# Performance work log

Measured on AMD Instinct MI355X. Metric: run time of the kernel, lower is better.

Reference implementation:

```python
import jax, jax.numpy as jnp
import numpy as np

EMBED = 512
HEADS = 8
HEAD_DIM = EMBED // HEADS


def setup_inputs() -> dict:
    key = jax.random.key(0)
    ks = jax.random.split(key, 11)
    B, S, E = 2, 4096, EMBED
    scale = 1.0 / np.sqrt(E)
    inp = {
        "q": jax.random.normal(ks[0], (B, S, E), dtype=jnp.float32),
        "k": jax.random.normal(ks[1], (B, S, E), dtype=jnp.float32),
        "v": jax.random.normal(ks[2], (B, S, E), dtype=jnp.float32),
        # linear layer params (torch nn.Linear: y = x @ W.T + b)
        "Wq": jax.random.normal(ks[3], (E, E), dtype=jnp.float32) * scale,
        "bq": jnp.zeros((E,), dtype=jnp.float32),
        "Wk": jax.random.normal(ks[4], (E, E), dtype=jnp.float32) * scale,
        "bk": jnp.zeros((E,), dtype=jnp.float32),
        "Wv": jax.random.normal(ks[5], (E, E), dtype=jnp.float32) * scale,
        "bv": jnp.zeros((E,), dtype=jnp.float32),
        "Wo": jax.random.normal(ks[6], (E, E), dtype=jnp.float32) * scale,
        "bo": jnp.zeros((E,), dtype=jnp.float32),
    }
    return inp


def reference(q, k, v, Wq, bq, Wk, bk, Wv, bv, Wo, bo):
    B, Sq, E = q.shape
    Sk = k.shape[1]
    H, D = HEADS, HEAD_DIM
    # projections, split heads: [B, S, H, D]
    qh = (q @ Wq.T + bq).reshape(B, Sq, H, D)
    kh = (k @ Wk.T + bk).reshape(B, Sk, H, D)
    vh = (v @ Wv.T + bv).reshape(B, Sk, H, D)
    # full score matrix [B, H, Sq, Sk]; note: scaled by sqrt(embed_size), matching source
    scores = jnp.einsum('bqhe,bkhe->bhqk', qh, kh) / jnp.sqrt(jnp.float32(E))
    probs = jax.nn.softmax(scores, axis=-1)
    attn = jnp.einsum('bhql,blhd->bqhd', probs, vh)  # [B, Sq, H, D]
    concat = attn.reshape(B, Sq, E)
    return concat @ Wo.T + bo
```

## Files before the change

kernel.cpp:

```cpp
#include <hip/hip_runtime.h>
#include <hip/hip_bf16.h>

#define DEVFN __device__ __forceinline__

typedef __attribute__((ext_vector_type(8))) __bf16 bf16x8;
typedef __attribute__((ext_vector_type(4))) float f32x4;
typedef __attribute__((ext_vector_type(16))) float f32x16;

constexpr int E  = 512;
constexpr int S  = 4096;
constexpr int HD = 64;
constexpr int RT = 8192;

DEVFN unsigned int cvt_pk_bf16(float lo, float hi) {
  unsigned int r;
  asm("v_cvt_pk_bf16_f32 %0, %1, %2" : "=v"(r) : "v"(lo), "v"(hi));
  return r;
}
DEVFN void plswap(unsigned int& a, unsigned int& b) {
  asm("v_permlane32_swap_b32 %0, %1" : "+v"(a), "+v"(b));
}
DEVFN float ex2(float x) { return __builtin_amdgcn_exp2f(x); }

DEVFN unsigned short f2bf(float f) {
  union { float f; unsigned int u; } v; v.f = f;
  unsigned int u = v.u;
  return (unsigned short)((u + 0x7fffu + ((u >> 16) & 1u)) >> 16);
}

DEVFN f32x4 mfma16(bf16x8 a, bf16x8 b, f32x4 c) {
  return __builtin_amdgcn_mfma_f32_16x16x32_bf16(a, b, c, 0, 0, 0);
}
DEVFN f32x16 mfma32(bf16x8 a, bf16x8 b, f32x16 c) {
  return __builtin_amdgcn_mfma_f32_32x32x16_bf16(a, b, c, 0, 0, 0);
}

DEVFN uint4 pk8(const float4& a, const float4& b) {
  uint4 r;
  r.x = cvt_pk_bf16(a.x, a.y); r.y = cvt_pk_bf16(a.z, a.w);
  r.z = cvt_pk_bf16(b.x, b.y); r.w = cvt_pk_bf16(b.z, b.w);
  return r;
}
DEVFN bf16x8 asbf(uint4 u) { union { uint4 a; bf16x8 b; } c; c.a = u; return c.b; }

template<typename TIN, int OMODE>
DEVFN void gemm_body(const TIN* __restrict__ X, const float* __restrict__ W,
                     const float* __restrict__ bias, void* __restrict__ outp,
                     float scale, unsigned short (*Al)[72], unsigned short (*Bl)[72]) {
  const int bid0 = blockIdx.x;
  const int bid = ((bid0 & 7) << 5) | (bid0 >> 3);
  const int bm = bid >> 2, bn = bid & 3;
  const int tid = threadIdx.x;
  const int w = tid >> 6, lane = tid & 63;
  const int g = lane >> 4, ln = lane & 15;
  const int wm = w >> 2, wn = w & 3;
  const int r0 = bm * 128, n0 = bn * 128;
  const int srw = tid >> 2, sc0 = (tid & 3) * 16;

  f32x4 acc[4][2] = {};

  float4 af[4];
  uint4  au[2];
  float4 bp[4];

  auto loadA = [&](int k0) {
    if constexpr (sizeof(TIN) == 4) {
      const float* src = (const float*)X + (size_t)(r0 + srw) * E + k0 + sc0;
      #pragma unroll
      for (int i = 0; i < 4; ++i) af[i] = *(const float4*)(src + i * 4);
    } else {
      const unsigned short* src = (const unsigned short*)X + (size_t)(r0 + srw) * E + k0 + sc0;
      #pragma unroll
      for (int i = 0; i < 2; ++i) au[i] = *(const uint4*)(src + i * 8);
    }
  };
  auto loadB = [&](int k0) {
    const float* src = W + (size_t)(n0 + srw) * E + k0 + sc0;
    #pragma unroll
    for (int i = 0; i < 4; ++i) bp[i] = *(const float4*)(src + i * 4);
  };

  loadA(0); loadB(0);

  for (int k0 = 0; k0 < E; k0 += 64) {
    if constexpr (sizeof(TIN) == 4) {
      *(uint4*)&Al[srw][sc0]     = pk8(af[0], af[1]);
      *(uint4*)&Al[srw][sc0 + 8] = pk8(af[2], af[3]);
    } else {
      *(uint4*)&Al[srw][sc0]     = au[0];
      *(uint4*)&Al[srw][sc0 + 8] = au[1];
    }
    *(uint4*)&Bl[srw][sc0]     = pk8(bp[0], bp[1]);
    *(uint4*)&Bl[srw][sc0 + 8] = pk8(bp[2], bp[3]);
    __syncthreads();
    if (k0 + 64 < E) { loadA(k0 + 64); loadB(k0 + 64); }

    __builtin_amdgcn_s_setprio(1);
    #pragma unroll
    for (int kk = 0; kk < 2; ++kk) {
      bf16x8 afr[4], bfr[2];
      #pragma unroll
      for (int i = 0; i < 4; ++i)
        afr[i] = *(const bf16x8*)&Al[wm*64 + i*16 + ln][kk*32 + 8*g];
      #pragma unroll
      for (int j = 0; j < 2; ++j)
        bfr[j] = *(const bf16x8*)&Bl[wn*32 + j*16 + ln][kk*32 + 8*g];
      #pragma unroll
      for (int i = 0; i < 4; ++i)
        #pragma unroll
        for (int j = 0; j < 2; ++j)
          acc[i][j] = mfma16(afr[i], bfr[j], acc[i][j]);
    }
    __builtin_amdgcn_s_setprio(0);
    __syncthreads();
  }

  #pragma unroll
  for (int j = 0; j < 2; ++j) {
    const int gcol = n0 + wn*32 + j*16 + ln;
    const float bv = bias[gcol];
    #pragma unroll
    for (int i = 0; i < 4; ++i) {
      const int gr = r0 + wm*64 + i*16 + 4*g;
      #pragma unroll
      for (int r = 0; r < 4; ++r) {
        const float v = (acc[i][j][r] + bv) * scale;
        if constexpr (OMODE == 1)
          ((float*)outp)[(size_t)(gr + r) * E + gcol] = v;
        else if constexpr (OMODE == 0)
          ((unsigned short*)outp)[(size_t)(gr + r) * E + gcol] = f2bf(v);
        else
          ((unsigned short*)outp)[((size_t)((gr + r) >> 12) * E + gcol) * S + ((gr + r) & (S - 1))] = f2bf(v);
      }
    }
  }
}

__global__ __launch_bounds__(512) void gemm_qkv(const float* __restrict__ q,
    const float* __restrict__ k, const float* __restrict__ v,
    const float* __restrict__ Wq, const float* __restrict__ bq,
    const float* __restrict__ Wk, const float* __restrict__ bk,
    const float* __restrict__ Wv, const float* __restrict__ bv,
    unsigned short* qh, unsigned short* kh, unsigned short* vhT, float qscale) {
  __shared__ unsigned short Al[128][72];
  __shared__ unsigned short Bl[128][72];
  const int y = blockIdx.y;
  if (y == 0)      gemm_body<float, 0>(q, Wq, bq, qh, qscale, Al, Bl);
  else if (y == 1) gemm_body<float, 0>(k, Wk, bk, kh, 1.0f, Al, Bl);
  else             gemm_body<float, 2>(v, Wv, bv, vhT, 1.0f, Al, Bl);
}

__global__ __launch_bounds__(512) void gemm_o(const unsigned short* __restrict__ cc,
    const float* __restrict__ Wo, const float* __restrict__ bo, float* out) {
  __shared__ unsigned short Al[128][72];
  __shared__ unsigned short Bl[128][72];
  gemm_body<unsigned short, 1>(cc, Wo, bo, out, 1.0f, Al, Bl);
}

__global__ __launch_bounds__(512) void attn_fwd(const unsigned short* __restrict__ qh,
                                                const unsigned short* __restrict__ kh,
                                                const unsigned short* __restrict__ vhT,
                                                unsigned short* __restrict__ cc) {
  __shared__ unsigned short SM[4][64][72];

  const int bid = blockIdx.x;
  const int swz = (bid & 7) * 64 + (bid >> 3);
  const int bh = swz >> 5, qt = swz & 31;
  const int b = bh >> 3, h = bh & 7;

  const int tid = threadIdx.x;
  const int wv = tid >> 6, lane = tid & 63;
  const int half = wv >> 2, w4 = wv & 3;
  const int l31 = lane & 31, hi = lane >> 5;

  unsigned short (*K_lds)[72] = SM[2*half];
  unsigned short (*V_lds)[72] = SM[2*half + 1];

  const unsigned short* qb = qh + (size_t)b * S * E + h * HD;
  const unsigned short* kb = kh + (size_t)b * S * E + h * HD;
  const unsigned short* vb = vhT + ((size_t)b * E + h * HD) * S;
  const int q0 = qt * 128 + w4 * 32;
  const int tbase = half * (S / 2);

  bf16x8 qf[4];
  #pragma unroll
  for (int kf = 0; kf < 4; ++kf)
    qf[kf] = *(const bf16x8*)(qb + (size_t)(q0 + l31) * E + kf*16 + 8*hi);

  f32x16 o0 = {}, o1 = {};
  float ml = -__builtin_inff(), ll = 0.f;

  const int t256 = tid & 255;
  const int srow = t256 >> 2, sc0 = (t256 & 3) * 16;
  const unsigned short* kS = kb + (size_t)(tbase + srow) * E + sc0;
  const unsigned short* vS = vb + (size_t)srow * S + tbase + sc0;

  uint4 kr0 = *(const uint4*)kS, kr1 = *(const uint4*)(kS + 8);
  uint4 vr0 = *(const uint4*)vS, vr1 = *(const uint4*)(vS + 8);

  constexpr int NIT = S / 2 / 64;
  for (int it = 0; it < NIT; ++it) {
    *(uint4*)&K_lds[srow][sc0]     = kr0;
    *(uint4*)&K_lds[srow][sc0 + 8] = kr1;
    *(uint4*)&V_lds[srow][sc0]     = vr0;
    *(uint4*)&V_lds[srow][sc0 + 8] = vr1;
    __syncthreads();

    if (it + 1 < NIT) {
      const unsigned short* kp = kS + (size_t)(it + 1) * 64 * E;
      const unsigned short* vp = vS + (it + 1) * 64;
      kr0 = *(const uint4*)kp; kr1 = *(const uint4*)(kp + 8);
      vr0 = *(const uint4*)vp; vr1 = *(const uint4*)(vp + 8);
    }

    f32x16 s0 = {}, s1 = {};
    __builtin_amdgcn_s_setprio(1);
    #pragma unroll
    for (int kf = 0; kf < 4; ++kf) {
      bf16x8 ka = *(const bf16x8*)&K_lds[l31]     [kf*16 + 8*hi];
      bf16x8 kc = *(const bf16x8*)&K_lds[32 + l31][kf*16 + 8*hi];
      s0 = mfma32(ka, qf[kf], s0);
      s1 = mfma32(kc, qf[kf], s1);
    }
    __builtin_amdgcn_s_setprio(0);

    float tm = -__builtin_inff();
    #pragma unroll
    for (int r = 0; r < 16; ++r) tm = fmaxf(tm, fmaxf(s0[r], s1[r]));
    tm = fmaxf(tm, __shfl_xor(tm, 32));

    if (!__all(tm <= ml + 8.f)) {
      const float mn = fmaxf(ml, tm);
      const float fr = ex2(ml - mn);
      ml = mn; ll *= fr;
      #pragma unroll
      for (int r = 0; r < 16; ++r) { o0[r] *= fr; o1[r] *= fr; }
    }

    float rs = 0.f;
    #pragma unroll
    for (int r = 0; r < 16; ++r) {
      s0[r] = ex2(s0[r] - ml); rs += s0[r];
      s1[r] = ex2(s1[r] - ml); rs += s1[r];
    }
    rs += __shfl_xor(rs, 32);
    ll += rs;

    unsigned int a0 = cvt_pk_bf16(s0[0],  s0[1]),  a1 = cvt_pk_bf16(s0[2],  s0[3]);
    unsigned int a2 = cvt_pk_bf16(s0[4],  s0[5]),  a3 = cvt_pk_bf16(s0[6],  s0[7]);
    unsigned int a4 = cvt_pk_bf16(s0[8],  s0[9]),  a5 = cvt_pk_bf16(s0[10], s0[11]);
    unsigned int a6 = cvt_pk_bf16(s0[12], s0[13]), a7 = cvt_pk_bf16(s0[14], s0[15]);
    plswap(a0, a2); plswap(a1, a3); plswap(a4, a6); plswap(a5, a7);
    unsigned int c0 = cvt_pk_bf16(s1[0],  s1[1]),  c1 = cvt_pk_bf16(s1[2],  s1[3]);
    unsigned int c2 = cvt_pk_bf16(s1[4],  s1[5]),  c3 = cvt_pk_bf16(s1[6],  s1[7]);
    unsigned int c4 = cvt_pk_bf16(s1[8],  s1[9]),  c5 = cvt_pk_bf16(s1[10], s1[11]);
    unsigned int c6 = cvt_pk_bf16(s1[12], s1[13]), c7 = cvt_pk_bf16(s1[14], s1[15]);
    plswap(c0, c2); plswap(c1, c3); plswap(c4, c6); plswap(c5, c7);
    uint4 pa[4];
    pa[0] = uint4{a0, a1, a2, a3};
    pa[1] = uint4{a4, a5, a6, a7};
    pa[2] = uint4{c0, c1, c2, c3};
    pa[3] = uint4{c4, c5, c6, c7};

    __builtin_amdgcn_s_setprio(1);
    #pragma unroll
    for (int tf = 0; tf < 4; ++tf) {
      bf16x8 va = *(const bf16x8*)&V_lds[l31]     [tf*16 + 8*hi];
      bf16x8 vc = *(const bf16x8*)&V_lds[32 + l31][tf*16 + 8*hi];
      bf16x8 pf = asbf(pa[tf]);
      o0 = mfma32(va, pf, o0);
      o1 = mfma32(vc, pf, o1);
    }
    __builtin_amdgcn_s_setprio(0);
    __syncthreads();
  }

  float* cb = (float*)SM;
  float* p = cb + (size_t)(w4 * 64 + lane) * 34;
  if (half) {
    #pragma unroll
    for (int r = 0; r < 16; ++r) { p[r] = o0[r]; p[16 + r] = o1[r]; }
    p[32] = ml; p[33] = ll;
  }
  __syncthreads();
  if (!half) {
    const float m2 = p[32], l2 = p[33];
    const float m = fmaxf(ml, m2);
    const float f1 = ex2(ml - m), f2 = ex2(m2 - m);
    ll = ll * f1 + l2 * f2;
    #pragma unroll
    for (int r = 0; r < 16; ++r) {
      o0[r] = o0[r] * f1 + p[r] * f2;
      o1[r] = o1[r] * f1 + p[16 + r] * f2;
    }

    const float inv = 1.0f / ll;
    const size_t rowb = (size_t)(b * S + q0 + l31) * E + h * HD;
    #pragma unroll
    for (int qd = 0; qd < 4; ++qd) {
      uint2 w0, w1;
      w0.x = cvt_pk_bf16(o0[4*qd]     * inv, o0[4*qd + 1] * inv);
      w0.y = cvt_pk_bf16(o0[4*qd + 2] * inv, o0[4*qd + 3] * inv);
      *(uint2*)&cc[rowb + 8*qd + 4*hi] = w0;
      w1.x = cvt_pk_bf16(o1[4*qd]     * inv, o1[4*qd + 1] * inv);
      w1.y = cvt_pk_bf16(o1[4*qd + 2] * inv, o1[4*qd + 3] * inv);
      *(uint2*)&cc[rowb + 32 + 8*qd + 4*hi] = w1;
    }
  }
}

extern "C" void kernel_launch(void* const* d_in, const int* in_sizes, int n_in,
                              void* d_out, int out_size, void* d_ws, size_t ws_size,
                              hipStream_t stream) {
  const float* q  = (const float*)d_in[0];
  const float* k  = (const float*)d_in[1];
  const float* v  = (const float*)d_in[2];
  const float* Wq = (const float*)d_in[3];
  const float* bq = (const float*)d_in[4];
  const float* Wk = (const float*)d_in[5];
  const float* bk = (const float*)d_in[6];
  const float* Wv = (const float*)d_in[7];
  const float* bv = (const float*)d_in[8];
  const float* Wo = (const float*)d_in[9];
  const float* bo = (const float*)d_in[10];
  float* out = (float*)d_out;

  unsigned short* qh  = (unsigned short*)d_ws;
  unsigned short* kh  = qh + (size_t)RT * E;
  unsigned short* vhT = kh + (size_t)RT * E;
  unsigned short* cc  = vhT + (size_t)RT * E;

  const float qscale = 1.4426950408889634f / 22.62741699796952f;

  gemm_qkv<<<dim3(256, 3), dim3(512), 0, stream>>>(q, k, v, Wq, bq, Wk, bk, Wv, bv,
                                                   qh, kh, vhT, qscale);
  attn_fwd<<<dim3(512), dim3(512), 0, stream>>>(qh, kh, vhT, cc);
  gemm_o<<<dim3(256), dim3(512), 0, stream>>>(cc, Wo, bo, out);
}
```

Before: 144.0 us.

## Split KV tile into 32-key subtiles and fold max subtraction into MFMA accumulator init

```diff
diff --git a/kernel.cpp b/kernel.cpp
--- a/kernel.cpp
+++ b/kernel.cpp
@@ -188,7 +188,8 @@
     qf[kf] = *(const bf16x8*)(qb + (size_t)(q0 + l31) * E + kf*16 + 8*hi);
 
   f32x16 o0 = {}, o1 = {};
-  float ml = -__builtin_inff(), ll = 0.f;
+  f32x16 cml = {};
+  float ml = 0.f, ll = 0.f;
 
   const int t256 = tid & 255;
   const int srow = t256 >> 2, sc0 = (t256 & 3) * 16;
@@ -213,65 +214,67 @@
       vr0 = *(const uint4*)vp; vr1 = *(const uint4*)(vp + 8);
     }
 
-    f32x16 s0 = {}, s1 = {};
-    __builtin_amdgcn_s_setprio(1);
-    #pragma unroll
-    for (int kf = 0; kf < 4; ++kf) {
-      bf16x8 ka = *(const bf16x8*)&K_lds[l31]     [kf*16 + 8*hi];
-      bf16x8 kc = *(const bf16x8*)&K_lds[32 + l31][kf*16 + 8*hi];
-      s0 = mfma32(ka, qf[kf], s0);
-      s1 = mfma32(kc, qf[kf], s1);
-    }
-    __builtin_amdgcn_s_setprio(0);
-
-    float tm = -__builtin_inff();
-    #pragma unroll
-    for (int r = 0; r < 16; ++r) tm = fmaxf(tm, fmaxf(s0[r], s1[r]));
-    tm = fmaxf(tm, __shfl_xor(tm, 32));
-
-    if (!__all(tm <= ml + 8.f)) {
-      const float mn = fmaxf(ml, tm);
-      const float fr = ex2(ml - mn);
-      ml = mn; ll *= fr;
-      #pragma unroll
-      for (int r = 0; r < 16; ++r) { o0[r] *= fr; o1[r] *= fr; }
-    }
-
-    float rs = 0.f;
-    #pragma unroll
-    for (int r = 0; r < 16; ++r) {
-      s0[r] = ex2(s0[r] - ml); rs += s0[r];
-      s1[r] = ex2(s1[r] - ml); rs += s1[r];
-    }
-    rs += __shfl_xor(rs, 32);
-    ll += rs;
-
-    unsigned int a0 = cvt_pk_bf16(s0[0],  s0[1]),  a1 = cvt_pk_bf16(s0[2],  s0[3]);
-    unsigned int a2 = cvt_pk_bf16(s0[4],  s0[5]),  a3 = cvt_pk_bf16(s0[6],  s0[7]);
-    unsigned int a4 = cvt_pk_bf16(s0[8],  s0[9]),  a5 = cvt_pk_bf16(s0[10], s0[11]);
-    unsigned int a6 = cvt_pk_bf16(s0[12], s0[13]), a7 = cvt_pk_bf16(s0[14], s0[15]);
-    plswap(a0, a2); plswap(a1, a3); plswap(a4, a6); plswap(a5, a7);
-    unsigned int c0 = cvt_pk_bf16(s1[0],  s1[1]),  c1 = cvt_pk_bf16(s1[2],  s1[3]);
-    unsigned int c2 = cvt_pk_bf16(s1[4],  s1[5]),  c3 = cvt_pk_bf16(s1[6],  s1[7]);
-    unsigned int c4 = cvt_pk_bf16(s1[8],  s1[9]),  c5 = cvt_pk_bf16(s1[10], s1[11]);
-    unsigned int c6 = cvt_pk_bf16(s1[12], s1[13]), c7 = cvt_pk_bf16(s1[14], s1[15]);
-    plswap(c0, c2); plswap(c1, c3); plswap(c4, c6); plswap(c5, c7);
-    uint4 pa[4];
-    pa[0] = uint4{a0, a1, a2, a3};
-    pa[1] = uint4{a4, a5, a6, a7};
-    pa[2] = uint4{c0, c1, c2, c3};
-    pa[3] = uint4{c4, c5, c6, c7};
-
-    __builtin_amdgcn_s_setprio(1);
-    #pragma unroll
-    for (int tf = 0; tf < 4; ++tf) {
-      bf16x8 va = *(const bf16x8*)&V_lds[l31]     [tf*16 + 8*hi];
-      bf16x8 vc = *(const bf16x8*)&V_lds[32 + l31][tf*16 + 8*hi];
-      bf16x8 pf = asbf(pa[tf]);
-      o0 = mfma32(va, pf, o0);
-      o1 = mfma32(vc, pf, o1);
-    }
-    __builtin_amdgcn_s_setprio(0);
+    #pragma unroll
+    for (int sub = 0; sub < 2; ++sub) {
+      const int koff = sub * 32;
+
+      f32x16 s;
+      __builtin_amdgcn_s_setprio(1);
+      {
+        bf16x8 k0 = *(const bf16x8*)&K_lds[koff + l31][8*hi];
+        s = mfma32(k0, qf[0], cml);
+        #pragma unroll
+        for (int kf = 1; kf < 4; ++kf) {
+          bf16x8 ka = *(const bf16x8*)&K_lds[koff + l31][kf*16 + 8*hi];
+          s = mfma32(ka, qf[kf], s);
+        }
+      }
+      __builtin_amdgcn_s_setprio(0);
+
+      float m0 = fmaxf(fmaxf(s[0],  s[1]),  s[2]);
+      float m1 = fmaxf(fmaxf(s[3],  s[4]),  s[5]);
+      float m2 = fmaxf(fmaxf(s[6],  s[7]),  s[8]);
+      float m3 = fmaxf(fmaxf(s[9],  s[10]), s[11]);
+      float m4 = fmaxf(fmaxf(s[12], s[13]), s[14]);
+      float tm = fmaxf(fmaxf(m0, m1), m2);
+      tm = fmaxf(fmaxf(tm, m3), fmaxf(m4, s[15]));
+      tm = fmaxf(tm, __shfl_xor(tm, 32));
+
+      if (!__all(tm <= 8.f)) {
+        const float delta = fmaxf(tm, 0.f);
+        const float fr = ex2(-delta);
+        ml += delta; ll *= fr;
+        #pragma unroll
+        for (int r = 0; r < 16; ++r) { o0[r] *= fr; o1[r] *= fr; s[r] -= delta; }
+        #pragma unroll
+        for (int r = 0; r < 16; ++r) cml[r] = -ml;
+      }
+
+      float rs = 0.f;
+      #pragma unroll
+      for (int r = 0; r < 16; ++r) { s[r] = ex2(s[r]); rs += s[r]; }
+      rs += __shfl_xor(rs, 32);
+      ll += rs;
+
+      unsigned int a0 = cvt_pk_bf16(s[0],  s[1]),  a1 = cvt_pk_bf16(s[2],  s[3]);
+      unsigned int a2 = cvt_pk_bf16(s[4],  s[5]),  a3 = cvt_pk_bf16(s[6],  s[7]);
+      unsigned int a4 = cvt_pk_bf16(s[8],  s[9]),  a5 = cvt_pk_bf16(s[10], s[11]);
+      unsigned int a6 = cvt_pk_bf16(s[12], s[13]), a7 = cvt_pk_bf16(s[14], s[15]);
+      plswap(a0, a2); plswap(a1, a3); plswap(a4, a6); plswap(a5, a7);
+      uint4 pa0 = uint4{a0, a1, a2, a3};
+      uint4 pa1 = uint4{a4, a5, a6, a7};
+
+      __builtin_amdgcn_s_setprio(1);
+      #pragma unroll
+      for (int tf = 0; tf < 2; ++tf) {
+        bf16x8 va = *(const bf16x8*)&V_lds[l31]     [koff + tf*16 + 8*hi];
+        bf16x8 vc = *(const bf16x8*)&V_lds[32 + l31][koff + tf*16 + 8*hi];
+        bf16x8 pf = asbf(tf ? pa1 : pa0);
+        o0 = mfma32(va, pf, o0);
+        o1 = mfma32(vc, pf, o1);
+      }
+      __builtin_amdgcn_s_setprio(0);
+    }
     __syncthreads();
   }
 
```

Result: slower. 147.7 us (+2.6%).
